# Optimization experiments

Measured on AMD Instinct MI355X. Metric: run time of the kernel, lower is better.

## Reference

```python
import jax, jax.numpy as jnp
import numpy as np

N_NODES = 100000
N_EDGES = 1600000
N_GRAPHS = 4096
HID = 512
OUT_DIM = 12


def setup_inputs() -> dict:
    key = jax.random.key(0)
    ks = jax.random.split(key, 16)
    x = jax.random.normal(ks[0], (N_NODES, 7), dtype=jnp.float32)
    edge_index = jax.random.randint(ks[1], (2, N_EDGES), 0, N_NODES, dtype=jnp.int32)
    batch = jnp.sort(jax.random.randint(ks[2], (N_NODES,), 0, N_GRAPHS, dtype=jnp.int32))

    def lin(k, i, o):
        s = 1.0 / np.sqrt(i)
        kw, kb = jax.random.split(k)
        return (jax.random.uniform(kw, (i, o), jnp.float32, -s, s),
                jax.random.uniform(kb, (o,), jnp.float32, -s, s))

    c1_w1, c1_b1 = lin(ks[3], 7, HID)
    c1_w2, c1_b2 = lin(ks[4], HID, HID)
    c2_w1, c2_b1 = lin(ks[5], HID, HID)
    c2_w2, c2_b2 = lin(ks[6], HID, HID)
    c3_w1, c3_b1 = lin(ks[7], HID, HID)
    c3_w2, c3_b2 = lin(ks[8], HID, HID)
    lin_w1, lin_b1 = lin(ks[9], HID, 256)
    lin_w2, lin_b2 = lin(ks[10], 256, OUT_DIM)
    return dict(x=x, edge_index=edge_index, batch=batch,
                c1_w1=c1_w1, c1_b1=c1_b1, c1_w2=c1_w2, c1_b2=c1_b2,
                c2_w1=c2_w1, c2_b1=c2_b1, c2_w2=c2_w2, c2_b2=c2_b2,
                c3_w1=c3_w1, c3_b1=c3_b1, c3_w2=c3_w2, c3_b2=c3_b2,
                lin_w1=lin_w1, lin_b1=lin_b1, lin_w2=lin_w2, lin_b2=lin_b2)


def _gin_conv(x, src, dst, w1, b1, w2, b2):
    # GINConv (eps=0): h_i = mlp(x_i + sum_{j in N(i)} x_j)
    agg = jax.ops.segment_sum(x[src], dst, num_segments=N_NODES)
    h = x + agg
    h = jax.nn.relu(h @ w1 + b1) @ w2 + b2
    return h


def reference(x, edge_index, batch,
              c1_w1, c1_b1, c1_w2, c1_b2,
              c2_w1, c2_b1, c2_w2, c2_b2,
              c3_w1, c3_b1, c3_w2, c3_b2,
              lin_w1, lin_b1, lin_w2, lin_b2):
    src, dst = edge_index[0], edge_index[1]
    h = jax.nn.relu(_gin_conv(x, src, dst, c1_w1, c1_b1, c1_w2, c1_b2))
    h = jax.nn.relu(_gin_conv(h, src, dst, c2_w1, c2_b1, c2_w2, c2_b2))
    h = jax.nn.relu(_gin_conv(h, src, dst, c3_w1, c3_b1, c3_w2, c3_b2))
    # global mean pool over graphs in batch
    sums = jax.ops.segment_sum(h, batch, num_segments=N_GRAPHS)
    cnts = jax.ops.segment_sum(jnp.ones((h.shape[0],), h.dtype), batch, num_segments=N_GRAPHS)
    pooled = sums / jnp.maximum(cnts, 1.0)[:, None]
    return jax.nn.relu(pooled @ lin_w1 + lin_b1) @ lin_w2 + lin_b2
```

## Files before the change

### kernel.cpp

```cpp
#include <hip/hip_runtime.h>
#include <hip/hip_bf16.h>
#include <cstddef>
#include <cstdint>

#define N_NODES   100000
#define M_PAD     100096
#define N_EDGES   1600000
#define N_GRAPHS  4096
#define HID       512
#define OUT_DIM   12

typedef unsigned short u16;
typedef __attribute__((ext_vector_type(8))) short bf16x8;
typedef __attribute__((ext_vector_type(4))) float f32x4;

__device__ inline float bf2f(u16 u) {
    union { uint32_t i; float f; } v; v.i = (uint32_t)u << 16; return v.f;
}
__device__ inline u16 f2bf(float f) {
    union { float f; uint32_t i; } v; v.f = f;
    uint32_t r = v.i + 0x7FFFu + ((v.i >> 16) & 1u);
    return (u16)(r >> 16);
}

__device__ inline void load8_bf(const u16* p, float o[8]) {
    uint4 u = *(const uint4*)p;
    uint32_t w[4] = {u.x, u.y, u.z, u.w};
    #pragma unroll
    for (int i = 0; i < 4; ++i) {
        o[2*i]   = bf2f((u16)(w[i] & 0xFFFFu));
        o[2*i+1] = bf2f((u16)(w[i] >> 16));
    }
}
__device__ inline void store8_bf(u16* p, const float o[8]) {
    uint4 u;
    u.x = (uint32_t)f2bf(o[0]) | ((uint32_t)f2bf(o[1]) << 16);
    u.y = (uint32_t)f2bf(o[2]) | ((uint32_t)f2bf(o[3]) << 16);
    u.z = (uint32_t)f2bf(o[4]) | ((uint32_t)f2bf(o[5]) << 16);
    u.w = (uint32_t)f2bf(o[6]) | ((uint32_t)f2bf(o[7]) << 16);
    *(uint4*)p = u;
}

__device__ inline void gld16(const void* g, void* l) {
    __builtin_amdgcn_global_load_lds(
        (const __attribute__((address_space(1))) void*)g,
        (__attribute__((address_space(3))) void*)(uint32_t)(uintptr_t)l,
        16, 0, 0);
}

__global__ void zero_ints(int* __restrict__ p, int n) {
    int i = blockIdx.x * blockDim.x + threadIdx.x;
    if (i < n) p[i] = 0;
}

__global__ void hist_kernel(const int* __restrict__ dst, int* __restrict__ counts) {
    int e = blockIdx.x * blockDim.x + threadIdx.x;
    if (e < N_EDGES) atomicAdd(&counts[dst[e]], 1);
}

#define SCAN_NB 98

__global__ __launch_bounds__(1024) void scan_chunks(const int* __restrict__ counts,
                                                    int* __restrict__ row_start,
                                                    int* __restrict__ partials) {
    __shared__ int smem[1024];
    int tid = threadIdx.x;
    int i = blockIdx.x * 1024 + tid;
    int v = (i < N_NODES) ? counts[i] : 0;
    smem[tid] = v;
    __syncthreads();
    for (int off = 1; off < 1024; off <<= 1) {
        int t = (tid >= off) ? smem[tid - off] : 0;
        __syncthreads();
        smem[tid] += t;
        __syncthreads();
    }
    if (i < N_NODES) row_start[i + 1] = smem[tid];
    if (tid == 1023) partials[blockIdx.x] = smem[1023];
}

__global__ void scan_partials(int* __restrict__ partials) {
    if (threadIdx.x == 0 && blockIdx.x == 0) {
        int run = 0;
        for (int b = 0; b < SCAN_NB; ++b) {
            int t = partials[b];
            partials[b] = run;
            run += t;
        }
    }
}

__global__ __launch_bounds__(1024) void scan_add_offsets(int* __restrict__ row_start,
                                                         const int* __restrict__ partials) {
    int i = blockIdx.x * 1024 + threadIdx.x;
    if (i == 0) row_start[0] = 0;
    if (i < N_NODES) row_start[i + 1] += partials[blockIdx.x];
}

__global__ void cursor_init(const int* __restrict__ row_start, int* __restrict__ cursor) {
    int i = blockIdx.x * blockDim.x + threadIdx.x;
    if (i < N_NODES) cursor[i] = row_start[i];
}

__global__ void scatter_edges(const int* __restrict__ src, const int* __restrict__ dst,
                              int* __restrict__ cursor, int* __restrict__ sorted_src) {
    int e = blockIdx.x * blockDim.x + threadIdx.x;
    if (e < N_EDGES) {
        int p = atomicAdd(&cursor[dst[e]], 1);
        p = min(max(p, 0), N_EDGES - 1);
        sorted_src[p] = src[e];
    }
}

__global__ __launch_bounds__(256) void transpose_to_bf16(const float* __restrict__ W,
                                                         u16* __restrict__ Wt) {
    __shared__ float t[32][33];
    int bx = blockIdx.x * 32, by = blockIdx.y * 32;
    int tx = threadIdx.x & 31, ty = threadIdx.x >> 5;
    #pragma unroll
    for (int i = 0; i < 32; i += 8)
        t[ty + i][tx] = W[(size_t)(by + ty + i) * HID + bx + tx];
    __syncthreads();
    #pragma unroll
    for (int i = 0; i < 32; i += 8)
        Wt[(size_t)(bx + ty + i) * HID + by + tx] = f2bf(t[tx][ty + i]);
}

template <int HALF>
__global__ __launch_bounds__(256) void agg_half(const u16* __restrict__ X,
                                                const int* __restrict__ row_start,
                                                const int* __restrict__ sorted_src,
                                                u16* __restrict__ Out) {
    int node = blockIdx.x * 4 + (threadIdx.x >> 6);
    int lane = threadIdx.x & 63;
    size_t col = HALF * 256 + lane * 4;
    uint2 s = *(const uint2*)(X + (size_t)node * HID + col);
    float a0 = bf2f((u16)(s.x & 0xFFFFu)), a1 = bf2f((u16)(s.x >> 16));
    float a2 = bf2f((u16)(s.y & 0xFFFFu)), a3 = bf2f((u16)(s.y >> 16));
    int e0 = min(row_start[node], N_EDGES);
    int e1 = min(row_start[node + 1], N_EDGES);
    for (int e = e0; e < e1; ++e) {
        unsigned si = min((unsigned)sorted_src[e], (unsigned)(N_NODES - 1));
        uint2 v = *(const uint2*)(X + (size_t)si * HID + col);
        a0 += bf2f((u16)(v.x & 0xFFFFu)); a1 += bf2f((u16)(v.x >> 16));
        a2 += bf2f((u16)(v.y & 0xFFFFu)); a3 += bf2f((u16)(v.y >> 16));
    }
    uint2 o;
    o.x = (uint32_t)f2bf(a0) | ((uint32_t)f2bf(a1) << 16);
    o.y = (uint32_t)f2bf(a2) | ((uint32_t)f2bf(a3) << 16);
    unsigned long long packed = (unsigned long long)o.x | ((unsigned long long)o.y << 32);
    __builtin_nontemporal_store(packed,
        (unsigned long long*)(Out + (size_t)node * HID + col));
}

__global__ __launch_bounds__(64) void agg7_kernel(const float* __restrict__ x,
                                                  const int* __restrict__ row_start,
                                                  const int* __restrict__ sorted_src,
                                                  float* __restrict__ out) {
    int node = blockIdx.x * 8 + (threadIdx.x >> 3);
    int d = threadIdx.x & 7;
    if (node >= N_NODES || d >= 7) return;
    float acc = x[(size_t)node * 7 + d];
    int e0 = min(row_start[node], N_EDGES);
    int e1 = min(row_start[node + 1], N_EDGES);
    for (int e = e0; e < e1; ++e) {
        unsigned si = min((unsigned)sorted_src[e], (unsigned)(N_NODES - 1));
        acc += x[(size_t)si * 7 + d];
    }
    out[(size_t)node * 7 + d] = acc;
}

__global__ __launch_bounds__(256) void gemm_k7_relu(const float* __restrict__ A7,
                                                    const float* __restrict__ W,
                                                    const float* __restrict__ bias,
                                                    u16* __restrict__ C) {
    __shared__ float Wl[7 * HID];
    __shared__ float Bi[HID];
    __shared__ float A7l[128 * 7];
    int tid = threadIdx.x;
    int node0 = blockIdx.x * 128;
    for (int t = tid; t < 7 * HID; t += 256) Wl[t] = W[t];
    for (int t = tid; t < HID; t += 256) Bi[t] = bias[t];
    for (int t = tid; t < 128 * 7; t += 256) {
        int gi = node0 * 7 + t;
        A7l[t] = (gi < N_NODES * 7) ? A7[gi] : 0.f;
    }
    __syncthreads();
    int wid = tid >> 6, lane = tid & 63;
    for (int it = 0; it < 32; ++it) {
        int nl = it * 4 + wid;
        int node = node0 + nl;
        if (node >= N_NODES) break;
        float a[7];
        #pragma unroll
        for (int k = 0; k < 7; ++k) a[k] = A7l[nl * 7 + k];
        float s[8];
        int c0 = lane * 8;
        #pragma unroll
        for (int c = 0; c < 8; ++c) {
            float v = Bi[c0 + c];
            #pragma unroll
            for (int k = 0; k < 7; ++k) v = fmaf(a[k], Wl[k * HID + c0 + c], v);
            s[c] = fmaxf(v, 0.f);
        }
        store8_bf(C + (size_t)node * HID + c0, s);
    }
}

template <bool RELU>
__global__ __launch_bounds__(256) void gemm_mfma_bf16(const u16* __restrict__ A,
                                                      const u16* __restrict__ Wt,
                                                      const float* __restrict__ bias,
                                                      u16* __restrict__ C) {
    __shared__ u16 As[128][32];
    __shared__ u16 Bs[128][32];
    const int tid  = threadIdx.x;
    const int wid  = tid >> 6;
    const int lane = tid & 63;
    const int wr = wid >> 1, wc = wid & 1;
    const int row0 = blockIdx.y * 128;
    const int col0 = blockIdx.x * 128;
    const int l15 = lane & 15;
    const int l4  = lane >> 4;

    const int srow = lane >> 2;
    const int scol = (lane & 3) * 8;

    f32x4 acc[4][4] = {};

    for (int k0 = 0; k0 < HID; k0 += 32) {
        const u16* Ag = A  + (size_t)(row0 + wid * 32) * HID + k0;
        const u16* Bg = Wt + (size_t)(col0 + wid * 32) * HID + k0;
        #pragma unroll
        for (int i = 0; i < 2; ++i) {
            gld16(Ag + (size_t)(i * 16 + srow) * HID + scol, &As[wid * 32 + i * 16][0]);
            gld16(Bg + (size_t)(i * 16 + srow) * HID + scol, &Bs[wid * 32 + i * 16][0]);
        }
        __syncthreads();
        bf16x8 af[4], bfr[4];
        #pragma unroll
        for (int m = 0; m < 4; ++m)
            af[m] = *(const bf16x8*)&As[wr * 64 + m * 16 + l15][l4 * 8];
        #pragma unroll
        for (int n = 0; n < 4; ++n)
            bfr[n] = *(const bf16x8*)&Bs[wc * 64 + n * 16 + l15][l4 * 8];
        #pragma unroll
        for (int m = 0; m < 4; ++m)
            #pragma unroll
            for (int n = 0; n < 4; ++n)
                acc[m][n] = __builtin_amdgcn_mfma_f32_16x16x32_bf16(af[m], bfr[n],
                                                                    acc[m][n], 0, 0, 0);
        __syncthreads();
    }

    #pragma unroll
    for (int m = 0; m < 4; ++m) {
        #pragma unroll
        for (int n = 0; n < 4; ++n) {
            int col = col0 + wc * 64 + n * 16 + l15;
            float b = bias[col];
            #pragma unroll
            for (int i = 0; i < 4; ++i) {
                int r = row0 + wr * 64 + m * 16 + l4 * 4 + i;
                float v = acc[m][n][i] + b;
                if (RELU) v = fmaxf(v, 0.f);
                C[(size_t)r * HID + col] = f2bf(v);
            }
        }
    }
}

template <bool RELU>
__global__ __launch_bounds__(256) void gemm_tiled_f32(const float* __restrict__ A,
                                                      const float* __restrict__ W,
                                                      const float* __restrict__ bias,
                                                      float* __restrict__ C,
                                                      int M, int N, int K) {
    __shared__ float As[16][68];
    __shared__ float Bs[16][68];
    int tid = threadIdx.x;
    int tx = tid & 15, ty = tid >> 4;
    int col0 = blockIdx.x * 64;
    int row0 = blockIdx.y * 64;
    float acc[4][4] = {};

    for (int k0 = 0; k0 < K; k0 += 16) {
        {
            int r = tid >> 2, c = (tid & 3) * 4;
            float4 v = make_float4(0.f, 0.f, 0.f, 0.f);
            int gr = row0 + r;
            if (gr < M) v = *reinterpret_cast<const float4*>(A + (size_t)gr * K + k0 + c);
            As[c + 0][r] = v.x; As[c + 1][r] = v.y; As[c + 2][r] = v.z; As[c + 3][r] = v.w;
        }
        {
            int r = tid >> 4, c = (tid & 15) * 4;
            int gc = col0 + c;
            float4 v = make_float4(0.f, 0.f, 0.f, 0.f);
            const float* wp = W + (size_t)(k0 + r) * N + gc;
            if (gc + 3 < N) {
                v = *reinterpret_cast<const float4*>(wp);
            } else {
                float t0 = (gc + 0 < N) ? wp[0] : 0.f;
                float t1 = (gc + 1 < N) ? wp[1] : 0.f;
                float t2 = (gc + 2 < N) ? wp[2] : 0.f;
                v = make_float4(t0, t1, t2, 0.f);
            }
            *reinterpret_cast<float4*>(&Bs[r][c]) = v;
        }
        __syncthreads();
        #pragma unroll
        for (int k = 0; k < 16; ++k) {
            float a[4], b[4];
            *(float4*)a = *(const float4*)&As[k][ty * 4];
            *(float4*)b = *(const float4*)&Bs[k][tx * 4];
            #pragma unroll
            for (int i = 0; i < 4; ++i)
                #pragma unroll
                for (int j = 0; j < 4; ++j)
                    acc[i][j] = fmaf(a[i], b[j], acc[i][j]);
        }
        __syncthreads();
    }

    #pragma unroll
    for (int i = 0; i < 4; ++i) {
        int r = row0 + ty * 4 + i;
        if (r >= M) break;
        #pragma unroll
        for (int j = 0; j < 4; ++j) {
            int cidx = col0 + tx * 4 + j;
            if (cidx >= N) continue;
            float v = acc[i][j] + bias[cidx];
            if (RELU) v = fmaxf(v, 0.f);
            C[(size_t)r * N + cidx] = v;
        }
    }
}

__global__ void graph_bounds(const int* __restrict__ batch, int* __restrict__ g_start) {
    int g = blockIdx.x * blockDim.x + threadIdx.x;
    if (g > N_GRAPHS) return;
    int lo = 0, hi = N_NODES;
    while (lo < hi) {
        int mid = (lo + hi) >> 1;
        if (batch[mid] < g) lo = mid + 1; else hi = mid;
    }
    g_start[g] = lo;
}

__global__ __launch_bounds__(256) void pool_kernel(const u16* __restrict__ H,
                                                   const int* __restrict__ g_start,
                                                   float* __restrict__ pooled) {
    int g = blockIdx.x * 4 + (threadIdx.x >> 6);
    if (g >= N_GRAPHS) return;
    int lane = threadIdx.x & 63;
    int s = g_start[g], e = g_start[g + 1];
    float acc[8] = {};
    for (int n = s; n < e; ++n) {
        float v[8];
        load8_bf(H + (size_t)n * HID + lane * 8, v);
        #pragma unroll
        for (int k = 0; k < 8; ++k) acc[k] += v[k];
    }
    float inv = 1.f / fmaxf((float)(e - s), 1.f);
    float* o = pooled + (size_t)g * HID + lane * 8;
    #pragma unroll
    for (int k = 0; k < 8; ++k) o[k] = acc[k] * inv;
}

__global__ void diag_kernel(float* __restrict__ out, int n, float v) {
    int i = blockIdx.x * blockDim.x + threadIdx.x;
    if (i < n) out[i] = v;
}

static inline size_t rnd256(size_t b) { return (b + 255) & ~(size_t)255; }

extern "C" void kernel_launch(void* const* d_in, const int* in_sizes, int n_in,
                              void* d_out, int out_size, void* d_ws, size_t ws_size,
                              hipStream_t stream) {
    (void)in_sizes; (void)n_in;
    const float* x     = (const float*)d_in[0];
    const int*   ei    = (const int*)d_in[1];
    const int*   batch = (const int*)d_in[2];
    const int* src = ei;
    const int* dst = ei + N_EDGES;

    const float* c1_w1 = (const float*)d_in[3];
    const float* c1_b1 = (const float*)d_in[4];
    const float* c1_w2 = (const float*)d_in[5];
    const float* c1_b2 = (const float*)d_in[6];
    const float* c2_w1 = (const float*)d_in[7];
    const float* c2_b1 = (const float*)d_in[8];
    const float* c2_w2 = (const float*)d_in[9];
    const float* c2_b2 = (const float*)d_in[10];
    const float* c3_w1 = (const float*)d_in[11];
    const float* c3_b1 = (const float*)d_in[12];
    const float* c3_w2 = (const float*)d_in[13];
    const float* c3_b2 = (const float*)d_in[14];
    const float* lin_w1 = (const float*)d_in[15];
    const float* lin_b1 = (const float*)d_in[16];
    const float* lin_w2 = (const float*)d_in[17];
    const float* lin_b2 = (const float*)d_in[18];
    float* out = (float*)d_out;

    size_t off = 0;
    auto alloc = [&](size_t bytes) -> void* {
        void* p = (char*)d_ws + off;
        off += rnd256(bytes);
        return p;
    };
    u16*   b0        = (u16*)alloc((size_t)M_PAD * HID * 2);
    u16*   b1        = (u16*)alloc((size_t)M_PAD * HID * 2);
    float* agg7buf   = (float*)alloc((size_t)N_NODES * 7 * 4);
    int*   counts    = (int*)alloc((size_t)N_NODES * 4);
    int*   cursor    = (int*)alloc((size_t)N_NODES * 4);
    int*   row_start = (int*)alloc((size_t)(N_NODES + 1) * 4);
    int*   sorted_src= (int*)alloc((size_t)N_EDGES * 4);
    int*   g_start   = (int*)alloc((size_t)(N_GRAPHS + 1) * 4);
    int*   partials  = (int*)alloc((size_t)SCAN_NB * 4);
    float* pooled    = (float*)alloc((size_t)N_GRAPHS * HID * 4);
    char*  hh_slot   = (char*)alloc((size_t)N_GRAPHS * 256 * 4);
    float* hh        = (float*)hh_slot;
    u16*   wt        = (u16*)hh_slot;
    u16* c1w2T = wt + 0 * HID * HID;
    u16* c2w1T = wt + 1 * HID * HID;
    u16* c2w2T = wt + 2 * HID * HID;
    u16* c3w1T = wt + 3 * HID * HID;
    u16* c3w2T = wt + 4 * HID * HID;

    if (off > ws_size) {
        diag_kernel<<<(out_size + 255) / 256, 256, 0, stream>>>(
            out, out_size, (float)(ws_size >> 20));
        return;
    }

    zero_ints<<<(N_NODES + 255) / 256, 256, 0, stream>>>(counts, N_NODES);
    hist_kernel<<<(N_EDGES + 255) / 256, 256, 0, stream>>>(dst, counts);
    scan_chunks<<<SCAN_NB, 1024, 0, stream>>>(counts, row_start, partials);
    scan_partials<<<1, 64, 0, stream>>>(partials);
    scan_add_offsets<<<SCAN_NB, 1024, 0, stream>>>(row_start, partials);
    cursor_init<<<(N_NODES + 255) / 256, 256, 0, stream>>>(row_start, cursor);
    scatter_edges<<<(N_EDGES + 255) / 256, 256, 0, stream>>>(src, dst, cursor, sorted_src);
    graph_bounds<<<(N_GRAPHS + 256) / 256, 256, 0, stream>>>(batch, g_start);

    dim3 tgrid(HID / 32, HID / 32);
    transpose_to_bf16<<<tgrid, 256, 0, stream>>>(c1_w2, c1w2T);
    transpose_to_bf16<<<tgrid, 256, 0, stream>>>(c2_w1, c2w1T);
    transpose_to_bf16<<<tgrid, 256, 0, stream>>>(c2_w2, c2w2T);
    transpose_to_bf16<<<tgrid, 256, 0, stream>>>(c3_w1, c3w1T);
    transpose_to_bf16<<<tgrid, 256, 0, stream>>>(c3_w2, c3w2T);

    dim3 mgrid(HID / 128, M_PAD / 128);
    const int aggGrid = N_NODES / 4;

    agg7_kernel<<<(N_NODES + 7) / 8, 64, 0, stream>>>(x, row_start, sorted_src, agg7buf);
    gemm_k7_relu<<<(N_NODES + 127) / 128, 256, 0, stream>>>(agg7buf, c1_w1, c1_b1, b0);
    gemm_mfma_bf16<true><<<mgrid, 256, 0, stream>>>(b0, c1w2T, c1_b2, b1);
    agg_half<0><<<aggGrid, 256, 0, stream>>>(b1, row_start, sorted_src, b0);
    agg_half<1><<<aggGrid, 256, 0, stream>>>(b1, row_start, sorted_src, b0);
    gemm_mfma_bf16<true><<<mgrid, 256, 0, stream>>>(b0, c2w1T, c2_b1, b1);
    gemm_mfma_bf16<true><<<mgrid, 256, 0, stream>>>(b1, c2w2T, c2_b2, b0);
    agg_half<0><<<aggGrid, 256, 0, stream>>>(b0, row_start, sorted_src, b1);
    agg_half<1><<<aggGrid, 256, 0, stream>>>(b0, row_start, sorted_src, b1);
    gemm_mfma_bf16<true><<<mgrid, 256, 0, stream>>>(b1, c3w1T, c3_b1, b0);
    gemm_mfma_bf16<true><<<mgrid, 256, 0, stream>>>(b0, c3w2T, c3_b2, b1);
    pool_kernel<<<N_GRAPHS / 4, 256, 0, stream>>>(b1, g_start, pooled);
    gemm_tiled_f32<true><<<dim3(256 / 64, N_GRAPHS / 64), 256, 0, stream>>>(
        pooled, lin_w1, lin_b1, hh, N_GRAPHS, 256, HID);
    gemm_tiled_f32<false><<<dim3(1, N_GRAPHS / 64), 256, 0, stream>>>(
        hh, lin_w2, lin_b2, out, N_GRAPHS, OUT_DIM, 256);
}
```

Before: 1.613 ms.

## Merge half-row aggregation kernels into one full-row kernel handling two nodes per wave

```diff
diff --git a/kernel.cpp b/kernel.cpp
--- a/kernel.cpp
+++ b/kernel.cpp
@@ -39,6 +39,16 @@
     u.z = (uint32_t)f2bf(o[4]) | ((uint32_t)f2bf(o[5]) << 16);
     u.w = (uint32_t)f2bf(o[6]) | ((uint32_t)f2bf(o[7]) << 16);
     *(uint4*)p = u;
+}
+__device__ inline void store8_bf_nt(u16* p, const float o[8]) {
+    unsigned long long lo =
+        (unsigned long long)((uint32_t)f2bf(o[0]) | ((uint32_t)f2bf(o[1]) << 16)) |
+        ((unsigned long long)((uint32_t)f2bf(o[2]) | ((uint32_t)f2bf(o[3]) << 16)) << 32);
+    unsigned long long hi =
+        (unsigned long long)((uint32_t)f2bf(o[4]) | ((uint32_t)f2bf(o[5]) << 16)) |
+        ((unsigned long long)((uint32_t)f2bf(o[6]) | ((uint32_t)f2bf(o[7]) << 16)) << 32);
+    __builtin_nontemporal_store(lo, (unsigned long long*)p);
+    __builtin_nontemporal_store(hi, (unsigned long long*)(p + 4));
 }
 
 __device__ inline void gld16(const void* g, void* l) {
@@ -126,31 +136,45 @@
         Wt[(size_t)(bx + ty + i) * HID + by + tx] = f2bf(t[tx][ty + i]);
 }
 
-template <int HALF>
-__global__ __launch_bounds__(256) void agg_half(const u16* __restrict__ X,
-                                                const int* __restrict__ row_start,
-                                                const int* __restrict__ sorted_src,
-                                                u16* __restrict__ Out) {
-    int node = blockIdx.x * 4 + (threadIdx.x >> 6);
+__global__ __launch_bounds__(256) void agg_full2(const u16* __restrict__ X,
+                                                 const int* __restrict__ row_start,
+                                                 const int* __restrict__ sorted_src,
+                                                 u16* __restrict__ Out) {
+    int w    = threadIdx.x >> 6;
     int lane = threadIdx.x & 63;
-    size_t col = HALF * 256 + lane * 4;
-    uint2 s = *(const uint2*)(X + (size_t)node * HID + col);
-    float a0 = bf2f((u16)(s.x & 0xFFFFu)), a1 = bf2f((u16)(s.x >> 16));
-    float a2 = bf2f((u16)(s.y & 0xFFFFu)), a3 = bf2f((u16)(s.y >> 16));
-    int e0 = min(row_start[node], N_EDGES);
-    int e1 = min(row_start[node + 1], N_EDGES);
-    for (int e = e0; e < e1; ++e) {
-        unsigned si = min((unsigned)sorted_src[e], (unsigned)(N_NODES - 1));
-        uint2 v = *(const uint2*)(X + (size_t)si * HID + col);
-        a0 += bf2f((u16)(v.x & 0xFFFFu)); a1 += bf2f((u16)(v.x >> 16));
-        a2 += bf2f((u16)(v.y & 0xFFFFu)); a3 += bf2f((u16)(v.y >> 16));
-    }
-    uint2 o;
-    o.x = (uint32_t)f2bf(a0) | ((uint32_t)f2bf(a1) << 16);
-    o.y = (uint32_t)f2bf(a2) | ((uint32_t)f2bf(a3) << 16);
-    unsigned long long packed = (unsigned long long)o.x | ((unsigned long long)o.y << 32);
-    __builtin_nontemporal_store(packed,
-        (unsigned long long*)(Out + (size_t)node * HID + col));
+    int n0 = (blockIdx.x * 4 + w) * 2;
+    int n1 = n0 + 1;
+    size_t coff = (size_t)lane * 8;
+
+    float a0[8], a1[8];
+    load8_bf(X + (size_t)n0 * HID + coff, a0);
+    load8_bf(X + (size_t)n1 * HID + coff, a1);
+
+    int s0 = min(row_start[n0], N_EDGES);
+    int m0 = min(row_start[n0 + 1], N_EDGES);
+    int e1 = min(row_start[n1 + 1], N_EDGES);
+    int c0 = m0 - s0;
+    int c1 = e1 - m0;
+    int cm = max(c0, c1);
+
+    for (int t = 0; t < cm; ++t) {
+        if (t < c0) {
+            unsigned si = min((unsigned)sorted_src[s0 + t], (unsigned)(N_NODES - 1));
+            float v[8];
+            load8_bf(X + (size_t)si * HID + coff, v);
+            #pragma unroll
+            for (int k = 0; k < 8; ++k) a0[k] += v[k];
+        }
+        if (t < c1) {
+            unsigned si = min((unsigned)sorted_src[m0 + t], (unsigned)(N_NODES - 1));
+            float v[8];
+            load8_bf(X + (size_t)si * HID + coff, v);
+            #pragma unroll
+            for (int k = 0; k < 8; ++k) a1[k] += v[k];
+        }
+    }
+    store8_bf_nt(Out + (size_t)n0 * HID + coff, a0);
+    store8_bf_nt(Out + (size_t)n1 * HID + coff, a1);
 }
 
 __global__ __launch_bounds__(64) void agg7_kernel(const float* __restrict__ x,
@@ -451,17 +475,15 @@
     transpose_to_bf16<<<tgrid, 256, 0, stream>>>(c3_w2, c3w2T);
 
     dim3 mgrid(HID / 128, M_PAD / 128);
-    const int aggGrid = N_NODES / 4;
+    const int agg2Grid = N_NODES / 8;
 
     agg7_kernel<<<(N_NODES + 7) / 8, 64, 0, stream>>>(x, row_start, sorted_src, agg7buf);
     gemm_k7_relu<<<(N_NODES + 127) / 128, 256, 0, stream>>>(agg7buf, c1_w1, c1_b1, b0);
     gemm_mfma_bf16<true><<<mgrid, 256, 0, stream>>>(b0, c1w2T, c1_b2, b1);
-    agg_half<0><<<aggGrid, 256, 0, stream>>>(b1, row_start, sorted_src, b0);
-    agg_half<1><<<aggGrid, 256, 0, stream>>>(b1, row_start, sorted_src, b0);
+    agg_full2<<<agg2Grid, 256, 0, stream>>>(b1, row_start, sorted_src, b0);
     gemm_mfma_bf16<true><<<mgrid, 256, 0, stream>>>(b0, c2w1T, c2_b1, b1);
     gemm_mfma_bf16<true><<<mgrid, 256, 0, stream>>>(b1, c2w2T, c2_b2, b0);
-    agg_half<0><<<aggGrid, 256, 0, stream>>>(b0, row_start, sorted_src, b1);
-    agg_half<1><<<aggGrid, 256, 0, stream>>>(b0, row_start, sorted_src, b1);
+    agg_full2<<<agg2Grid, 256, 0, stream>>>(b0, row_start, sorted_src, b1);
     gemm_mfma_bf16<true><<<mgrid, 256, 0, stream>>>(b1, c3w1T, c3_b1, b0);
     gemm_mfma_bf16<true><<<mgrid, 256, 0, stream>>>(b0, c3w2T, c3_b2, b1);
     pool_kernel<<<N_GRAPHS / 4, 256, 0, stream>>>(b1, g_start, pooled);
```

Measured after the change: 1.414 ms. -12.4%, faster.
